# Optimization experiments

Hardware: AMD Instinct MI355X
Metric: run time of the kernel (lower is better)

Reference implementation:

```python
import jax, jax.numpy as jnp
import numpy as np

K = 16          # neighboursnum
NEG_SLOPE = 0.01  # torch LeakyReLU default
EPS = 1e-5      # torch BatchNorm default


def _bn(x, gamma, beta, axes):
    # BatchNorm in training mode: biased batch stats over `axes`, channel dim = 1
    mu = x.mean(axes, keepdims=True)
    var = x.var(axes, keepdims=True)
    shape = [1] * x.ndim
    shape[1] = -1
    return (x - mu) / jnp.sqrt(var + EPS) * gamma.reshape(shape) + beta.reshape(shape)


def _lrelu(x):
    return jnp.where(x >= 0, x, NEG_SLOPE * x)


def setup_inputs() -> dict:
    key = jax.random.key(0)
    ks = jax.random.split(key, 9)
    B, D, N, O = 4, 64, 4096, 128
    s = 0.05
    return {
        "f_in": jax.random.normal(ks[0], (B, D, N), jnp.float32),
        "w_local": jax.random.normal(ks[1], (O, 2 * D + 1), jnp.float32) * s,
        "g_local": jnp.ones((O,), jnp.float32),
        "b_local": jnp.zeros((O,), jnp.float32),
        "w_sem": jax.random.normal(ks[2], (O, D), jnp.float32) * s,
        "g_sem": jnp.ones((O,), jnp.float32),
        "b_sem": jnp.zeros((O,), jnp.float32),
        "w_full": jax.random.normal(ks[3], (O, 2 * O), jnp.float32) * s,
        "g_full": jnp.ones((O,), jnp.float32),
        "b_full": jnp.zeros((O,), jnp.float32),
        "wq": jax.random.normal(ks[4], (D, D), jnp.float32) * s,
        "bq": jax.random.normal(ks[5], (D,), jnp.float32) * s,
        "wk": jax.random.normal(ks[6], (D, D), jnp.float32) * s,
        "bk": jax.random.normal(ks[7], (D,), jnp.float32) * s,
        "wv": jax.random.normal(ks[8], (D, D), jnp.float32) * s,
        "bv": jax.random.normal(jax.random.fold_in(key, 99), (D,), jnp.float32) * s,
    }


def reference(f_in, w_local, g_local, b_local, w_sem, g_sem, b_sem,
              w_full, g_full, b_full, wq, bq, wk, bk, wv, bv):
    B, D, N = f_in.shape
    # --- knn on feature space: pairwise negative squared distance, topk ---
    xx = jnp.sum(f_in * f_in, axis=1)                       # (B,N)
    inner = jnp.einsum('bdm,bdn->bmn', f_in, f_in)          # (B,N,N)
    pd = -xx[:, :, None] + 2.0 * inner - xx[:, None, :]     # -||xi-xj||^2
    idx = jax.lax.top_k(pd, K)[1]                           # (B,N,K) nearest
    # --- gather graph feature ---
    x_t = jnp.swapaxes(f_in, 1, 2)                          # (B,N,D)
    neigh = x_t[jnp.arange(B)[:, None, None], idx]          # (B,N,K,D)
    central = jnp.broadcast_to(x_t[:, :, None, :], neigh.shape)
    dist = jnp.linalg.norm(neigh - central, axis=3, keepdims=True)  # (B,N,K,1)
    feat = jnp.concatenate([central, neigh, dist], axis=3)  # (B,N,K,2D+1)
    feat = jnp.transpose(feat, (0, 3, 1, 2))                # (B,2D+1,N,K)
    # --- localConv (1x1 conv2d, no bias) + BN2d + LeakyReLU, max over K ---
    intra = _lrelu(_bn(jnp.einsum('oc,bcnk->bonk', w_local, feat),
                       g_local, b_local, (0, 2, 3)))
    intra = intra.max(axis=-1)                              # (B,O,N)
    # --- self-attention over points ---
    q = jnp.einsum('od,bdn->bon', wq, f_in) + bq[None, :, None]
    k = jnp.einsum('od,bdn->bon', wk, f_in) + bk[None, :, None]
    v = jnp.einsum('od,bdn->bon', wv, f_in) + bv[None, :, None]
    scores = jax.nn.softmax(
        jnp.einsum('bdm,bdn->bmn', q, k) / jnp.sqrt(jnp.float32(D)), axis=-1)
    fgt = jnp.einsum('bmn,bdn->bdm', scores, v)             # (B,D,N)
    # --- semConv (1x1 conv1d) + BN1d + LeakyReLU ---
    inter = _lrelu(_bn(jnp.einsum('od,bdn->bon', w_sem, fgt),
                       g_sem, b_sem, (0, 2)))               # (B,O,N)
    # --- fullConv on concat ---
    cat = jnp.concatenate([intra, inter], axis=1)           # (B,2O,N)
    out = _lrelu(_bn(jnp.einsum('oc,bcn->bon', w_full, cat),
                     g_full, b_full, (0, 2)))               # (B,O,N)
    return out
```

## Files before the change

kernel.cpp:

```cpp
#include <hip/hip_runtime.h>
#include <math.h>

constexpr int NB = 4;
constexpr int ND = 64;
constexpr int NNN = 4096;
constexpr int NO = 128;
constexpr int NK = 16;
constexpr float NEG = 0.01f;
constexpr float BN_EPS = 1e-5f;

typedef unsigned short u16;
typedef unsigned int u32;
typedef __attribute__((ext_vector_type(8))) short short8;
typedef __attribute__((ext_vector_type(4))) float floatx4;

constexpr int OFF_XX    = 0;
constexpr int OFF_IDX   = 16384;
constexpr int OFF_D2    = 278528;
constexpr int OFF_Q     = 540672;
constexpr int OFF_K     = 1589248;
constexpr int OFF_V     = 2637824;
constexpr int OFF_FGT   = 3686400;
constexpr int OFF_APRE  = 4734976;
constexpr int OFF_BPRE  = 6832128;
constexpr int OFF_IMAX  = 8929280;
constexpr int OFF_IMIN  = 11026432;
constexpr int OFF_ZSEM  = OFF_Q;
constexpr int OFF_ZFULL = OFF_V;
constexpr int OFF_STATS = 13123584;
constexpr int OFF_COEF  = 13124352;
constexpr int OFF_LINV  = 13125120;

__device__ __forceinline__ u16 f2b(float x) {
  u32 u = __builtin_bit_cast(u32, x);
  u += 0x7fffu + ((u >> 16) & 1u);
  return (u16)(u >> 16);
}

template <int CTRL>
__device__ __forceinline__ float fmax_dpp(float v) {
  int b = __builtin_bit_cast(int, v);
  int s = __builtin_amdgcn_update_dpp(b, b, CTRL, 0xF, 0xF, false);
  return fmaxf(v, __builtin_bit_cast(float, s));
}
__device__ __forceinline__ void pairmax(float av, int ai, float bv, int bi, float& rv, int& ri) {
  bool tk = bv > av;
  rv = tk ? bv : av;
  ri = tk ? bi : ai;
}

__global__ void k_xx(const float* __restrict__ f, float* __restrict__ xx) {
  int gid = blockIdx.x * 256 + threadIdx.x;
  int b = gid >> 12, n = gid & 4095;
  const float* fb = f + b * ND * NNN + n;
  float s = 0.f;
#pragma unroll
  for (int d = 0; d < ND; ++d) { float v = fb[d * NNN]; s += v * v; }
  xx[gid] = s;
}

__global__ __launch_bounds__(256) void k_qkv(const float* __restrict__ f,
    const float* __restrict__ wq, const float* __restrict__ bq,
    const float* __restrict__ wk, const float* __restrict__ bk,
    const float* __restrict__ wv, const float* __restrict__ bv,
    u16* __restrict__ qb, u16* __restrict__ kb, u16* __restrict__ vb) {
  int sel = blockIdx.y;
  const float* W    = (sel == 0) ? wq : (sel == 1) ? wk : wv;
  const float* bias = (sel == 0) ? bq : (sel == 1) ? bk : bv;
  int t = threadIdx.x;
  int lane = t & 63;
  int og = __builtin_amdgcn_readfirstlane(t >> 6);
  int gcol = blockIdx.x * 64 + lane;
  int b = gcol >> 12, n = gcol & 4095;
  const float* fb = f + b * ND * NNN + n;
  float cv[64];
#pragma unroll
  for (int d = 0; d < ND; ++d) cv[d] = fb[d * NNN];
  float acc[16];
#pragma unroll 1
  for (int oi = 0; oi < 16; ++oi) {
    int o = og * 16 + oi;
    const float* wr = W + o * ND;
    float a = bias[o];
#pragma unroll
    for (int d = 0; d < ND; ++d) a += wr[d] * cv[d];
    acc[oi] = a;
  }
  if (sel == 2) {
#pragma unroll
    for (int oi = 0; oi < 16; ++oi)
      vb[(size_t)(b * ND + og * 16 + oi) * NNN + n] = f2b(acc[oi]);
  } else {
    short8 p0, p1;
#pragma unroll
    for (int oi = 0; oi < 8; ++oi) { p0[oi] = (short)f2b(acc[oi]); p1[oi] = (short)f2b(acc[8 + oi]); }
    u16* dst = (sel ? kb : qb) + (size_t)(b * NNN + n) * ND + og * 16;
    *(short8*)dst = p0;
    *(short8*)(dst + 8) = p1;
  }
}

__global__ __launch_bounds__(256, 4) void k_knn(const float* __restrict__ f, const float* __restrict__ xx,
                                                int* __restrict__ tidx, float* __restrict__ td2) {
  __shared__ __align__(16) float fm[ND * 8];
  __shared__ __align__(16) float sl[4 * 2048];
  int t = threadIdx.x;
  int lane = t & 63;
  int w = __builtin_amdgcn_readfirstlane(t >> 6);
  int b = blockIdx.x >> 9;
  int m0 = (blockIdx.x & 511) << 3;
  const float* fb = f + b * ND * NNN;
  { int e = t;       int d = e >> 3, r = e & 7; fm[e] = fb[d * NNN + m0 + r]; }
  { int e = t + 256; int d = e >> 3, r = e & 7; fm[e] = fb[d * NNN + m0 + r]; }
  __syncthreads();
  float lv[2][2];
  int   li[2][2];
#pragma unroll
  for (int h = 0; h < 2; ++h) {
    float acc[64];
#pragma unroll
    for (int i = 0; i < 64; ++i) acc[i] = 0.f;
    for (int d = 0; d < ND; ++d) {
      const float* frow = fb + d * NNN + h * 2048 + 4 * t;
      float4 v0 = *(const float4*)(frow);
      float4 v1 = *(const float4*)(frow + 1024);
      float4 r0 = *(const float4*)&fm[d * 8];
      float4 r1 = *(const float4*)&fm[d * 8 + 4];
      float va0[4] = {v0.x, v0.y, v0.z, v0.w};
      float va1[4] = {v1.x, v1.y, v1.z, v1.w};
      float rr[8]  = {r0.x, r0.y, r0.z, r0.w, r1.x, r1.y, r1.z, r1.w};
#pragma unroll
      for (int c2 = 0; c2 < 4; ++c2)
#pragma unroll
        for (int r = 0; r < 8; ++r) {
          acc[c2 * 8 + r]      += va0[c2] * rr[r];
          acc[32 + c2 * 8 + r] += va1[c2] * rr[r];
        }
    }
    {
      const float* xrow = xx + b * NNN + h * 2048 + 4 * t;
      float4 x0 = *(const float4*)(xrow);
      float4 x1 = *(const float4*)(xrow + 1024);
      float xa0[4] = {x0.x, x0.y, x0.z, x0.w};
      float xa1[4] = {x1.x, x1.y, x1.z, x1.w};
#pragma unroll
      for (int c2 = 0; c2 < 4; ++c2)
#pragma unroll
        for (int r = 0; r < 8; ++r) {
          acc[c2 * 8 + r]      = 2.f * acc[c2 * 8 + r]      - xa0[c2];
          acc[32 + c2 * 8 + r] = 2.f * acc[32 + c2 * 8 + r] - xa1[c2];
        }
    }
#pragma unroll
    for (int s = 0; s < 2; ++s) {
      __syncthreads();
#pragma unroll
      for (int r4 = 0; r4 < 4; ++r4) {
        int r = s * 4 + r4;
#pragma unroll
        for (int jj = 0; jj < 2; ++jj) {
          float4 w4;
          w4.x = acc[jj * 32 + 0 * 8 + r];
          w4.y = acc[jj * 32 + 1 * 8 + r];
          w4.z = acc[jj * 32 + 2 * 8 + r];
          w4.w = acc[jj * 32 + 3 * 8 + r];
          *(float4*)&sl[r4 * 2048 + jj * 1024 + 4 * t] = w4;
        }
      }
      __syncthreads();
      float vals[32];
#pragma unroll
      for (int i = 0; i < 32; ++i) vals[i] = sl[w * 2048 + i * 64 + lane];
      float gv[8]; int gi[8];
#pragma unroll
      for (int g = 0; g < 8; ++g) {
        float v0 = vals[g * 4]; int i0 = (g * 4) * 64 + lane;
#pragma unroll
        for (int k2 = 1; k2 < 4; ++k2)
          pairmax(v0, i0, vals[g * 4 + k2], (g * 4 + k2) * 64 + lane, v0, i0);
        gv[g] = v0; gi[g] = i0;
      }
      float t1v[4]; int t1i[4];
      float t2v[2]; int t2i[2];
      float lvv; int lii;
#pragma unroll
      for (int p = 0; p < 4; ++p) pairmax(gv[2 * p], gi[2 * p], gv[2 * p + 1], gi[2 * p + 1], t1v[p], t1i[p]);
#pragma unroll
      for (int q = 0; q < 2; ++q) pairmax(t1v[2 * q], t1i[2 * q], t1v[2 * q + 1], t1i[2 * q + 1], t2v[q], t2i[q]);
      pairmax(t2v[0], t2i[0], t2v[1], t2i[1], lvv, lii);
      float selv = 0.f; int seli = 0;
#pragma unroll 1
      for (int kx = 0; kx < NK; ++kx) {
        float W = lvv;
        W = fmax_dpp<0xB1>(W);
        W = fmax_dpp<0x4E>(W);
        W = fmax_dpp<0x124>(W);
        W = fmax_dpp<0x128>(W);
        W = fmaxf(W, __shfl_xor(W, 16));
        W = fmaxf(W, __shfl_xor(W, 32));
        unsigned long long mk = __ballot(lvv == W);
        int lw = (int)__ffsll(mk) - 1;
        int wcol = __builtin_amdgcn_readlane(lii, lw);
        if (lane == kx) { selv = W; seli = wcol; }
        int jw = wcol >> 6;
#pragma unroll
        for (int g = 0; g < 8; ++g)
          if (g == (jw >> 2)) {
#pragma unroll
            for (int k2 = 0; k2 < 4; ++k2)
              if (k2 == (jw & 3))
                vals[g * 4 + k2] = (lane == lw) ? -3.0e38f : vals[g * 4 + k2];
            float v0 = vals[g * 4]; int i0 = (g * 4) * 64 + lane;
#pragma unroll
            for (int k2 = 1; k2 < 4; ++k2)
              pairmax(v0, i0, vals[g * 4 + k2], (g * 4 + k2) * 64 + lane, v0, i0);
            gv[g] = v0; gi[g] = i0;
            int p = g >> 1;
            pairmax(gv[2 * p], gi[2 * p], gv[2 * p + 1], gi[2 * p + 1], t1v[p], t1i[p]);
            int q = p >> 1;
            pairmax(t1v[2 * q], t1i[2 * q], t1v[2 * q + 1], t1i[2 * q + 1], t2v[q], t2i[q]);
            pairmax(t2v[0], t2i[0], t2v[1], t2i[1], lvv, lii);
          }
      }
      lv[h][s] = selv; li[h][s] = h * 2048 + seli;
    }
  }
#pragma unroll
  for (int s = 0; s < 2; ++s) {
    int m = m0 + s * 4 + w;
    float xm = xx[b * NNN + m];
    float a   = lv[0][s]; int ai  = li[0][s];
    float bb2 = lv[1][s]; int bi2 = li[1][s];
    int cntB = 0, cntA = 0;
#pragma unroll
    for (int j = 0; j < 16; ++j) {
      float bj = __shfl(bb2, j);
      cntB += (bj > a) ? 1 : 0;
      float aj = __shfl(a, j);
      cntA += (aj >= bb2) ? 1 : 0;
    }
    if (lane < 16) {
      int base = (b * NNN + m) * NK;
      int rA = lane + cntB;
      int rB = lane + cntA;
      if (rA < NK) {
        float dd = xm - a;
        tidx[base + rA] = ai;
        td2[base + rA] = dd > 0.f ? dd : 0.f;
      }
      if (rB < NK) {
        float dd = xm - bb2;
        tidx[base + rB] = bi2;
        td2[base + rB] = dd > 0.f ? dd : 0.f;
      }
    }
  }
}

__global__ __launch_bounds__(256) void k_attn(const u16* __restrict__ qb,
                                              const u16* __restrict__ kb,
                                              const u16* __restrict__ vb,
                                              float* __restrict__ fgt,
                                              float* __restrict__ linv) {
  __shared__ __align__(16) u16 P[32 * 520];
  __shared__ float rsum[4][32];
  int t = threadIdx.x;
  int lane = t & 63;
  int w = __builtin_amdgcn_readfirstlane(t >> 6);
  int quad = lane >> 4;
  int l15 = lane & 15;
  int b = blockIdx.x >> 7;
  int m0 = (blockIdx.x & 127) << 5;
  const u16* qra = qb + (size_t)(b * NNN + m0 + l15) * ND + quad * 8;
  const u16* qrb = qb + (size_t)(b * NNN + m0 + 16 + l15) * ND + quad * 8;
  short8 qa0a = *(const short8*)(qra), qa1a = *(const short8*)(qra + 32);
  short8 qa0b = *(const short8*)(qrb), qa1b = *(const short8*)(qrb + 32);
  const u16* kbase = kb + (size_t)b * NNN * ND;
  const u16* vrow  = vb + (size_t)(b * ND + w * 16 + l15) * NNN;
  floatx4 c2a = {0.f, 0.f, 0.f, 0.f};
  floatx4 c2b = {0.f, 0.f, 0.f, 0.f};
  float rsa[4] = {0.f, 0.f, 0.f, 0.f};
  float rsb[4] = {0.f, 0.f, 0.f, 0.f};
#pragma unroll 1
  for (int it = 0; it < 8; ++it) {
    int nchunk = it * 512;
#pragma unroll 1
    for (int ct = 0; ct < 8; ++ct) {
      int cc0 = (w * 8 + ct) * 16;
      const u16* krow = kbase + (size_t)(nchunk + cc0 + l15) * ND + quad * 8;
      short8 kf0 = *(const short8*)(krow);
      short8 kf1 = *(const short8*)(krow + 32);
      floatx4 acca = {0.f, 0.f, 0.f, 0.f};
      acca = __builtin_amdgcn_mfma_f32_16x16x32_bf16(qa0a, kf0, acca, 0, 0, 0);
      acca = __builtin_amdgcn_mfma_f32_16x16x32_bf16(qa1a, kf1, acca, 0, 0, 0);
      floatx4 accb = {0.f, 0.f, 0.f, 0.f};
      accb = __builtin_amdgcn_mfma_f32_16x16x32_bf16(qa0b, kf0, accb, 0, 0, 0);
      accb = __builtin_amdgcn_mfma_f32_16x16x32_bf16(qa1b, kf1, accb, 0, 0, 0);
      int ccol = cc0 + l15;
#pragma unroll
      for (int r = 0; r < 4; ++r) {
        float ea = __expf(acca[r] * 0.125f);
        rsa[r] += ea;
        P[(quad * 4 + r) * 520 + ccol] = f2b(ea);
        float eb = __expf(accb[r] * 0.125f);
        rsb[r] += eb;
        P[(16 + quad * 4 + r) * 520 + ccol] = f2b(eb);
      }
    }
    __syncthreads();
    const u16* vp = vrow + nchunk + quad * 8;
#pragma unroll
    for (int kk = 0; kk < 16; ++kk) {
      short8 b2 = *(const short8*)(vp + kk * 32);
      short8 a2a = *(const short8*)&P[l15 * 520 + kk * 32 + quad * 8];
      short8 a2b = *(const short8*)&P[(16 + l15) * 520 + kk * 32 + quad * 8];
      c2a = __builtin_amdgcn_mfma_f32_16x16x32_bf16(a2a, b2, c2a, 0, 0, 0);
      c2b = __builtin_amdgcn_mfma_f32_16x16x32_bf16(a2b, b2, c2b, 0, 0, 0);
    }
    __syncthreads();
  }
#pragma unroll
  for (int r = 0; r < 4; ++r) {
    float va = rsa[r];
    va += __shfl_xor(va, 1); va += __shfl_xor(va, 2);
    va += __shfl_xor(va, 4); va += __shfl_xor(va, 8);
    rsa[r] = va;
    float vb2 = rsb[r];
    vb2 += __shfl_xor(vb2, 1); vb2 += __shfl_xor(vb2, 2);
    vb2 += __shfl_xor(vb2, 4); vb2 += __shfl_xor(vb2, 8);
    rsb[r] = vb2;
  }
  if (l15 == 0) {
#pragma unroll
    for (int r = 0; r < 4; ++r) {
      rsum[w][quad * 4 + r] = rsa[r];
      rsum[w][16 + quad * 4 + r] = rsb[r];
    }
  }
#pragma unroll
  for (int r = 0; r < 4; ++r) {
    fgt[(size_t)(b * NNN + m0 + quad * 4 + r) * ND + w * 16 + l15] = c2a[r];
    fgt[(size_t)(b * NNN + m0 + 16 + quad * 4 + r) * ND + w * 16 + l15] = c2b[r];
  }
  __syncthreads();
  if (t < 32) {
    float s = rsum[0][t] + rsum[1][t] + rsum[2][t] + rsum[3][t];
    linv[b * NNN + m0 + t] = 1.f / s;
  }
}

__global__ __launch_bounds__(256) void k_ab(const float* __restrict__ f, const float* __restrict__ wl,
                                            float* __restrict__ Apre, float* __restrict__ Bpre) {
  __shared__ float fl[ND * 64];
  int t = threadIdx.x;
  int b = blockIdx.x >> 6;
  int n0 = (blockIdx.x & 63) << 6;
  for (int e = t; e < ND * 64; e += 256) {
    int d = e >> 6, c = e & 63;
    fl[e] = f[b * ND * NNN + d * NNN + n0 + c];
  }
  __syncthreads();
  int lane = t & 63;
  int w = __builtin_amdgcn_readfirstlane(t >> 6);
#pragma unroll 1
  for (int g = 0; g < 8; ++g) {
    float acc[8] = {0, 0, 0, 0, 0, 0, 0, 0};
    int p0 = w * 64 + g * 8;
    for (int d = 0; d < ND; ++d) {
      float fv = fl[d * 64 + lane];
#pragma unroll
      for (int u = 0; u < 8; ++u) {
        int p = p0 + u;
        int o = p & 127, sel = p >> 7;
        acc[u] += wl[o * 129 + sel * 64 + d] * fv;
      }
    }
#pragma unroll
    for (int u = 0; u < 8; ++u) {
      int p = p0 + u;
      int o = p & 127, sel = p >> 7;
      float* outp = sel ? Bpre : Apre;
      outp[(b * NNN + n0 + lane) * NO + o] = acc[u];
    }
  }
}

__global__ __launch_bounds__(128) void k_intra(const float* __restrict__ Apre, const float* __restrict__ Bpre,
                                               const int* __restrict__ tidx, const float* __restrict__ td2,
                                               const float* __restrict__ wl, float* __restrict__ imax,
                                               float* __restrict__ imin, float* __restrict__ stats) {
  __shared__ int sidx[32 * NK];
  __shared__ float sdst[32 * NK];
  int t = threadIdx.x;
  int b = blockIdx.x >> 7;
  int n0 = (blockIdx.x & 127) << 5;
  for (int e = t; e < 32 * NK; e += 128) {
    int base = (b * NNN + n0 + (e >> 4)) * NK + (e & 15);
    sidx[e] = tidx[base];
    sdst[e] = sqrtf(td2[base]);
  }
  __syncthreads();
  int o = t;
  float w128 = wl[o * 129 + 128];
  float ssum = 0.f, ssq = 0.f;
  for (int c = 0; c < 32; ++c) {
    float a = Apre[(b * NNN + n0 + c) * NO + o];
    float mx = -3.4e38f, mn = 3.4e38f;
#pragma unroll
    for (int kx = 0; kx < NK; ++kx) {
      int id = sidx[c * NK + kx];
      float y = a + Bpre[(b * NNN + id) * NO + o] + w128 * sdst[c * NK + kx];
      mx = fmaxf(mx, y); mn = fminf(mn, y);
      ssum += y; ssq += y * y;
    }
    imax[(b * NO + o) * NNN + n0 + c] = mx;
    imin[(b * NO + o) * NNN + n0 + c] = mn;
  }
  atomicAdd(&stats[o], ssum);
  atomicAdd(&stats[NO + o], ssq);
}

__global__ __launch_bounds__(256) void k_sem(const float* __restrict__ fgt, const float* __restrict__ linv,
                                             const float* __restrict__ wsem, float* __restrict__ zsem) {
  __shared__ float fl[64 * 65];
  int t = threadIdx.x;
  int b = blockIdx.x >> 6;
  int n0 = (blockIdx.x & 63) << 6;
  for (int e = t; e < 64 * 64; e += 256) {
    int n = e >> 6, d = e & 63;
    fl[n * 65 + d] = fgt[(size_t)(b * NNN + n0 + n) * ND + d] * linv[b * NNN + n0 + n];
  }
  __syncthreads();
  int lane = t & 63;
  int ob = __builtin_amdgcn_readfirstlane((t >> 6) * 32);
#pragma unroll 1
  for (int g = 0; g < 4; ++g) {
    float acc[8] = {0, 0, 0, 0, 0, 0, 0, 0};
    for (int d = 0; d < ND; ++d) {
      float fv = fl[lane * 65 + d];
#pragma unroll
      for (int u = 0; u < 8; ++u) acc[u] += wsem[(ob + g * 8 + u) * ND + d] * fv;
    }
#pragma unroll
    for (int u = 0; u < 8; ++u)
      zsem[(b * NO + ob + g * 8 + u) * NNN + n0 + lane] = acc[u];
  }
}

__global__ void k_stats(const float* __restrict__ zz, float* __restrict__ sout) {
  int o = blockIdx.x, t = threadIdx.x;
  float s = 0.f, q = 0.f;
  for (int b2 = 0; b2 < NB; ++b2) {
    const float* p = zz + (size_t)(b2 * NO + o) * NNN;
    for (int n = t; n < NNN; n += 256) { float v = p[n]; s += v; q += v * v; }
  }
#pragma unroll
  for (int off = 32; off; off >>= 1) { s += __shfl_down(s, off); q += __shfl_down(q, off); }
  __shared__ float rs[4], rq[4];
  int lane = t & 63, w = t >> 6;
  if (lane == 0) { rs[w] = s; rq[w] = q; }
  __syncthreads();
  if (t == 0) {
    sout[o]      = rs[0] + rs[1] + rs[2] + rs[3];
    sout[NO + o] = rq[0] + rq[1] + rq[2] + rq[3];
  }
}

__global__ void k_fin(const float* __restrict__ stats, const float* __restrict__ g,
                      const float* __restrict__ be, float cnt_inv, float* __restrict__ coef) {
  int o = threadIdx.x;
  float mean = stats[o] * cnt_inv;
  float var = stats[NO + o] * cnt_inv - mean * mean;
  var = var > 0.f ? var : 0.f;
  float a = g[o] * rsqrtf(var + BN_EPS);
  coef[o] = a;
  coef[NO + o] = be[o] - mean * a;
}

__global__ __launch_bounds__(256) void k_full(const float* __restrict__ imax, const float* __restrict__ imin,
                                              const float* __restrict__ zsem, const float* __restrict__ wfull,
                                              const float* __restrict__ coef, float* __restrict__ zfull) {
  __shared__ float fl[2 * NO * 64];
  int t = threadIdx.x;
  int b = blockIdx.x >> 6;
  int n0 = (blockIdx.x & 63) << 6;
  for (int e = t; e < 2 * NO * 64; e += 256) {
    int c = e >> 6, col = e & 63;
    float aa, bb, x;
    if (c < NO) {
      aa = coef[c]; bb = coef[NO + c];
      const float* src = (aa >= 0.f) ? imax : imin;
      x = src[(b * NO + c) * NNN + n0 + col];
    } else {
      int c2 = c - NO;
      aa = coef[2 * NO + c2]; bb = coef[3 * NO + c2];
      x = zsem[(b * NO + c2) * NNN + n0 + col];
    }
    float y = aa * x + bb;
    fl[e] = (y >= 0.f) ? y : NEG * y;
  }
  __syncthreads();
  int lane = t & 63;
  int ob = __builtin_amdgcn_readfirstlane((t >> 6) * 32);
#pragma unroll 1
  for (int g = 0; g < 4; ++g) {
    float acc[8] = {0, 0, 0, 0, 0, 0, 0, 0};
    for (int c = 0; c < 2 * NO; ++c) {
      float fv = fl[c * 64 + lane];
#pragma unroll
      for (int u = 0; u < 8; ++u) acc[u] += wfull[(ob + g * 8 + u) * (2 * NO) + c] * fv;
    }
#pragma unroll
    for (int u = 0; u < 8; ++u)
      zfull[(b * NO + ob + g * 8 + u) * NNN + n0 + lane] = acc[u];
  }
}

__global__ void k_out(const float* __restrict__ zfull, const float* __restrict__ coef,
                      float* __restrict__ out) {
  int gid = blockIdx.x * 256 + threadIdx.x;
  int o = (gid >> 12) & 127;
  float y = coef[o] * zfull[gid] + coef[NO + o];
  out[gid] = (y >= 0.f) ? y : NEG * y;
}

extern "C" void kernel_launch(void* const* d_in, const int* in_sizes, int n_in,
                              void* d_out, int out_size, void* d_ws, size_t ws_size,
                              hipStream_t stream) {
  (void)in_sizes; (void)n_in; (void)out_size; (void)ws_size;
  const float* f       = (const float*)d_in[0];
  const float* w_local = (const float*)d_in[1];
  const float* g_local = (const float*)d_in[2];
  const float* b_local = (const float*)d_in[3];
  const float* w_sem   = (const float*)d_in[4];
  const float* g_sem   = (const float*)d_in[5];
  const float* b_sem   = (const float*)d_in[6];
  const float* w_full  = (const float*)d_in[7];
  const float* g_full  = (const float*)d_in[8];
  const float* b_full  = (const float*)d_in[9];
  const float* wq = (const float*)d_in[10];
  const float* bq = (const float*)d_in[11];
  const float* wk = (const float*)d_in[12];
  const float* bk = (const float*)d_in[13];
  const float* wv = (const float*)d_in[14];
  const float* bv = (const float*)d_in[15];
  float* Wp = (float*)d_ws;
  u16* qb16 = (u16*)(Wp + OFF_Q);
  u16* kb16 = (u16*)(Wp + OFF_K);
  u16* vb16 = (u16*)(Wp + OFF_V);

  hipMemsetAsync(Wp + OFF_STATS, 0, 2 * NO * sizeof(float), stream);
  k_xx  <<<NB * NNN / 256, 256, 0, stream>>>(f, Wp + OFF_XX);
  k_qkv <<<dim3(NB * NNN / 64, 3), 256, 0, stream>>>(f, wq, bq, wk, bk, wv, bv, qb16, kb16, vb16);
  k_knn <<<NB * (NNN / 8), 256, 0, stream>>>(f, Wp + OFF_XX, (int*)(Wp + OFF_IDX), Wp + OFF_D2);
  k_attn<<<NB * (NNN / 32), 256, 0, stream>>>(qb16, kb16, vb16, Wp + OFF_FGT, Wp + OFF_LINV);
  k_ab  <<<NB * (NNN / 64), 256, 0, stream>>>(f, w_local, Wp + OFF_APRE, Wp + OFF_BPRE);
  k_intra<<<NB * (NNN / 32), 128, 0, stream>>>(Wp + OFF_APRE, Wp + OFF_BPRE,
                                               (const int*)(Wp + OFF_IDX), Wp + OFF_D2,
                                               w_local, Wp + OFF_IMAX, Wp + OFF_IMIN, Wp + OFF_STATS);
  k_sem <<<NB * (NNN / 64), 256, 0, stream>>>(Wp + OFF_FGT, Wp + OFF_LINV, w_sem, Wp + OFF_ZSEM);
  k_stats<<<NO, 256, 0, stream>>>(Wp + OFF_ZSEM, Wp + OFF_STATS + 2 * NO);
  k_fin <<<1, NO, 0, stream>>>(Wp + OFF_STATS,          g_local, b_local,
                               1.f / (float)(NB * NNN * NK), Wp + OFF_COEF);
  k_fin <<<1, NO, 0, stream>>>(Wp + OFF_STATS + 2 * NO, g_sem, b_sem,
                               1.f / (float)(NB * NNN), Wp + OFF_COEF + 2 * NO);
  k_full<<<NB * (NNN / 64), 256, 0, stream>>>(Wp + OFF_IMAX, Wp + OFF_IMIN, Wp + OFF_ZSEM,
                                              w_full, Wp + OFF_COEF, Wp + OFF_ZFULL);
  k_stats<<<NO, 256, 0, stream>>>(Wp + OFF_ZFULL, Wp + OFF_STATS + 4 * NO);
  k_fin <<<1, NO, 0, stream>>>(Wp + OFF_STATS + 4 * NO, g_full, b_full,
                               1.f / (float)(NB * NNN), Wp + OFF_COEF + 4 * NO);
  k_out <<<NB * NO * NNN / 256, 256, 0, stream>>>(Wp + OFF_ZFULL, Wp + OFF_COEF + 4 * NO,
                                                  (float*)d_out);
}
```

Before: 650.3 us.

## Fuse BN stats into producer kernels, bf16 A/B precompute, merge QKV and fin launches

Several independent changes. The BN sum and sum-of-squares reductions for the sem and full convolutions move into the producing kernels through wave shuffles and atomics, which removes two k_stats launches and their extra reads of zsem and zfull. The two k_fin launches become a single k_fin2. k_qkv now loops over Q, K and V inside one block so each feature column is loaded once, at the cost of three times fewer blocks. Apre and Bpre are stored as bf16 to halve the gather traffic in k_intra, which adds rounding error to the local-branch activations.

```diff
diff --git a/kernel.cpp b/kernel.cpp
--- a/kernel.cpp
+++ b/kernel.cpp
@@ -36,6 +36,10 @@
   u += 0x7fffu + ((u >> 16) & 1u);
   return (u16)(u >> 16);
 }
+__device__ __forceinline__ float b2f(u16 h) {
+  u32 u = (u32)h << 16;
+  return __builtin_bit_cast(float, u);
+}
 
 template <int CTRL>
 __device__ __forceinline__ float fmax_dpp(float v) {
@@ -64,9 +68,6 @@
     const float* __restrict__ wk, const float* __restrict__ bk,
     const float* __restrict__ wv, const float* __restrict__ bv,
     u16* __restrict__ qb, u16* __restrict__ kb, u16* __restrict__ vb) {
-  int sel = blockIdx.y;
-  const float* W    = (sel == 0) ? wq : (sel == 1) ? wk : wv;
-  const float* bias = (sel == 0) ? bq : (sel == 1) ? bk : bv;
   int t = threadIdx.x;
   int lane = t & 63;
   int og = __builtin_amdgcn_readfirstlane(t >> 6);
@@ -76,27 +77,32 @@
   float cv[64];
 #pragma unroll
   for (int d = 0; d < ND; ++d) cv[d] = fb[d * NNN];
-  float acc[16];
-#pragma unroll 1
-  for (int oi = 0; oi < 16; ++oi) {
-    int o = og * 16 + oi;
-    const float* wr = W + o * ND;
-    float a = bias[o];
-#pragma unroll
-    for (int d = 0; d < ND; ++d) a += wr[d] * cv[d];
-    acc[oi] = a;
-  }
-  if (sel == 2) {
-#pragma unroll
-    for (int oi = 0; oi < 16; ++oi)
-      vb[(size_t)(b * ND + og * 16 + oi) * NNN + n] = f2b(acc[oi]);
-  } else {
-    short8 p0, p1;
-#pragma unroll
-    for (int oi = 0; oi < 8; ++oi) { p0[oi] = (short)f2b(acc[oi]); p1[oi] = (short)f2b(acc[8 + oi]); }
-    u16* dst = (sel ? kb : qb) + (size_t)(b * NNN + n) * ND + og * 16;
-    *(short8*)dst = p0;
-    *(short8*)(dst + 8) = p1;
+#pragma unroll 1
+  for (int sel = 0; sel < 3; ++sel) {
+    const float* W    = (sel == 0) ? wq : (sel == 1) ? wk : wv;
+    const float* bias = (sel == 0) ? bq : (sel == 1) ? bk : bv;
+    float acc[16];
+#pragma unroll 1
+    for (int oi = 0; oi < 16; ++oi) {
+      int o = og * 16 + oi;
+      const float* wr = W + o * ND;
+      float a = bias[o];
+#pragma unroll
+      for (int d = 0; d < ND; ++d) a += wr[d] * cv[d];
+      acc[oi] = a;
+    }
+    if (sel == 2) {
+#pragma unroll
+      for (int oi = 0; oi < 16; ++oi)
+        vb[(size_t)(b * ND + og * 16 + oi) * NNN + n] = f2b(acc[oi]);
+    } else {
+      short8 p0, p1;
+#pragma unroll
+      for (int oi = 0; oi < 8; ++oi) { p0[oi] = (short)f2b(acc[oi]); p1[oi] = (short)f2b(acc[8 + oi]); }
+      u16* dst = (sel ? kb : qb) + (size_t)(b * NNN + n) * ND + og * 16;
+      *(short8*)dst = p0;
+      *(short8*)(dst + 8) = p1;
+    }
   }
 }
 
@@ -350,7 +356,7 @@
 }
 
 __global__ __launch_bounds__(256) void k_ab(const float* __restrict__ f, const float* __restrict__ wl,
-                                            float* __restrict__ Apre, float* __restrict__ Bpre) {
+                                            u16* __restrict__ Apre, u16* __restrict__ Bpre) {
   __shared__ float fl[ND * 64];
   int t = threadIdx.x;
   int b = blockIdx.x >> 6;
@@ -379,13 +385,13 @@
     for (int u = 0; u < 8; ++u) {
       int p = p0 + u;
       int o = p & 127, sel = p >> 7;
-      float* outp = sel ? Bpre : Apre;
-      outp[(b * NNN + n0 + lane) * NO + o] = acc[u];
-    }
-  }
-}
-
-__global__ __launch_bounds__(128) void k_intra(const float* __restrict__ Apre, const float* __restrict__ Bpre,
+      u16* outp = sel ? Bpre : Apre;
+      outp[(size_t)(b * NNN + n0 + lane) * NO + o] = f2b(acc[u]);
+    }
+  }
+}
+
+__global__ __launch_bounds__(128) void k_intra(const u16* __restrict__ Apre, const u16* __restrict__ Bpre,
                                                const int* __restrict__ tidx, const float* __restrict__ td2,
                                                const float* __restrict__ wl, float* __restrict__ imax,
                                                float* __restrict__ imin, float* __restrict__ stats) {
@@ -404,12 +410,12 @@
   float w128 = wl[o * 129 + 128];
   float ssum = 0.f, ssq = 0.f;
   for (int c = 0; c < 32; ++c) {
-    float a = Apre[(b * NNN + n0 + c) * NO + o];
+    float a = b2f(Apre[(size_t)(b * NNN + n0 + c) * NO + o]);
     float mx = -3.4e38f, mn = 3.4e38f;
 #pragma unroll
     for (int kx = 0; kx < NK; ++kx) {
       int id = sidx[c * NK + kx];
-      float y = a + Bpre[(b * NNN + id) * NO + o] + w128 * sdst[c * NK + kx];
+      float y = a + b2f(Bpre[(size_t)(b * NNN + id) * NO + o]) + w128 * sdst[c * NK + kx];
       mx = fmaxf(mx, y); mn = fminf(mn, y);
       ssum += y; ssq += y * y;
     }
@@ -421,7 +427,8 @@
 }
 
 __global__ __launch_bounds__(256) void k_sem(const float* __restrict__ fgt, const float* __restrict__ linv,
-                                             const float* __restrict__ wsem, float* __restrict__ zsem) {
+                                             const float* __restrict__ wsem, float* __restrict__ zsem,
+                                             float* __restrict__ sout) {
   __shared__ float fl[64 * 65];
   int t = threadIdx.x;
   int b = blockIdx.x >> 6;
@@ -442,28 +449,34 @@
       for (int u = 0; u < 8; ++u) acc[u] += wsem[(ob + g * 8 + u) * ND + d] * fv;
     }
 #pragma unroll
-    for (int u = 0; u < 8; ++u)
-      zsem[(b * NO + ob + g * 8 + u) * NNN + n0 + lane] = acc[u];
-  }
-}
-
-__global__ void k_stats(const float* __restrict__ zz, float* __restrict__ sout) {
-  int o = blockIdx.x, t = threadIdx.x;
-  float s = 0.f, q = 0.f;
-  for (int b2 = 0; b2 < NB; ++b2) {
-    const float* p = zz + (size_t)(b2 * NO + o) * NNN;
-    for (int n = t; n < NNN; n += 256) { float v = p[n]; s += v; q += v * v; }
-  }
-#pragma unroll
-  for (int off = 32; off; off >>= 1) { s += __shfl_down(s, off); q += __shfl_down(q, off); }
-  __shared__ float rs[4], rq[4];
-  int lane = t & 63, w = t >> 6;
-  if (lane == 0) { rs[w] = s; rq[w] = q; }
-  __syncthreads();
-  if (t == 0) {
-    sout[o]      = rs[0] + rs[1] + rs[2] + rs[3];
-    sout[NO + o] = rq[0] + rq[1] + rq[2] + rq[3];
-  }
+    for (int u = 0; u < 8; ++u) {
+      int o = ob + g * 8 + u;
+      zsem[(b * NO + o) * NNN + n0 + lane] = acc[u];
+      float s = acc[u], q = acc[u] * acc[u];
+#pragma unroll
+      for (int off = 1; off < 64; off <<= 1) { s += __shfl_xor(s, off); q += __shfl_xor(q, off); }
+      if (lane == 0) { atomicAdd(&sout[o], s); atomicAdd(&sout[NO + o], q); }
+    }
+  }
+}
+
+__global__ void k_fin2(const float* __restrict__ stats,
+                       const float* __restrict__ g1, const float* __restrict__ be1, float ci1,
+                       const float* __restrict__ g2, const float* __restrict__ be2, float ci2,
+                       float* __restrict__ coef) {
+  int t = threadIdx.x;
+  int o = t & 127;
+  int which = t >> 7;
+  const float* st = stats + which * 2 * NO;
+  const float* g  = which ? g2 : g1;
+  const float* be = which ? be2 : be1;
+  float ci = which ? ci2 : ci1;
+  float mean = st[o] * ci;
+  float var = st[NO + o] * ci - mean * mean;
+  var = var > 0.f ? var : 0.f;
+  float a = g[o] * rsqrtf(var + BN_EPS);
+  coef[which * 2 * NO + o] = a;
+  coef[which * 2 * NO + NO + o] = be[o] - mean * a;
 }
 
 __global__ void k_fin(const float* __restrict__ stats, const float* __restrict__ g,
@@ -479,7 +492,8 @@
 
 __global__ __launch_bounds__(256) void k_full(const float* __restrict__ imax, const float* __restrict__ imin,
                                               const float* __restrict__ zsem, const float* __restrict__ wfull,
-                                              const float* __restrict__ coef, float* __restrict__ zfull) {
+                                              const float* __restrict__ coef, float* __restrict__ zfull,
+                                              float* __restrict__ sout) {
   __shared__ float fl[2 * NO * 64];
   int t = threadIdx.x;
   int b = blockIdx.x >> 6;
@@ -511,8 +525,14 @@
       for (int u = 0; u < 8; ++u) acc[u] += wfull[(ob + g * 8 + u) * (2 * NO) + c] * fv;
     }
 #pragma unroll
-    for (int u = 0; u < 8; ++u)
-      zfull[(b * NO + ob + g * 8 + u) * NNN + n0 + lane] = acc[u];
+    for (int u = 0; u < 8; ++u) {
+      int o = ob + g * 8 + u;
+      zfull[(b * NO + o) * NNN + n0 + lane] = acc[u];
+      float s = acc[u], q = acc[u] * acc[u];
+#pragma unroll
+      for (int off = 1; off < 64; off <<= 1) { s += __shfl_xor(s, off); q += __shfl_xor(q, off); }
+      if (lane == 0) { atomicAdd(&sout[o], s); atomicAdd(&sout[NO + o], q); }
+    }
   }
 }
 
@@ -548,25 +568,27 @@
   u16* qb16 = (u16*)(Wp + OFF_Q);
   u16* kb16 = (u16*)(Wp + OFF_K);
   u16* vb16 = (u16*)(Wp + OFF_V);
-
-  hipMemsetAsync(Wp + OFF_STATS, 0, 2 * NO * sizeof(float), stream);
+  u16* ap16 = (u16*)(Wp + OFF_APRE);
+  u16* bp16 = (u16*)(Wp + OFF_BPRE);
+
+  hipMemsetAsync(Wp + OFF_STATS, 0, 6 * NO * sizeof(float), stream);
   k_xx  <<<NB * NNN / 256, 256, 0, stream>>>(f, Wp + OFF_XX);
-  k_qkv <<<dim3(NB * NNN / 64, 3), 256, 0, stream>>>(f, wq, bq, wk, bk, wv, bv, qb16, kb16, vb16);
+  k_qkv <<<NB * NNN / 64, 256, 0, stream>>>(f, wq, bq, wk, bk, wv, bv, qb16, kb16, vb16);
   k_knn <<<NB * (NNN / 8), 256, 0, stream>>>(f, Wp + OFF_XX, (int*)(Wp + OFF_IDX), Wp + OFF_D2);
   k_attn<<<NB * (NNN / 32), 256, 0, stream>>>(qb16, kb16, vb16, Wp + OFF_FGT, Wp + OFF_LINV);
-  k_ab  <<<NB * (NNN / 64), 256, 0, stream>>>(f, w_local, Wp + OFF_APRE, Wp + OFF_BPRE);
-  k_intra<<<NB * (NNN / 32), 128, 0, stream>>>(Wp + OFF_APRE, Wp + OFF_BPRE,
+  k_ab  <<<NB * (NNN / 64), 256, 0, stream>>>(f, w_local, ap16, bp16);
+  k_intra<<<NB * (NNN / 32), 128, 0, stream>>>(ap16, bp16,
                                                (const int*)(Wp + OFF_IDX), Wp + OFF_D2,
                                                w_local, Wp + OFF_IMAX, Wp + OFF_IMIN, Wp + OFF_STATS);
-  k_sem <<<NB * (NNN / 64), 256, 0, stream>>>(Wp + OFF_FGT, Wp + OFF_LINV, w_sem, Wp + OFF_ZSEM);
-  k_stats<<<NO, 256, 0, stream>>>(Wp + OFF_ZSEM, Wp + OFF_STATS + 2 * NO);
-  k_fin <<<1, NO, 0, stream>>>(Wp + OFF_STATS,          g_local, b_local,
-                               1.f / (float)(NB * NNN * NK), Wp + OFF_COEF);
-  k_fin <<<1, NO, 0, stream>>>(Wp + OFF_STATS + 2 * NO, g_sem, b_sem,
-                               1.f / (float)(NB * NNN), Wp + OFF_COEF + 2 * NO);
+  k_sem <<<NB * (NNN / 64), 256, 0, stream>>>(Wp + OFF_FGT, Wp + OFF_LINV, w_sem, Wp + OFF_ZSEM,
+                                              Wp + OFF_STATS + 2 * NO);
+  k_fin2<<<1, 2 * NO, 0, stream>>>(Wp + OFF_STATS,
+                                   g_local, b_local, 1.f / (float)(NB * NNN * NK),
+                                   g_sem, b_sem, 1.f / (float)(NB * NNN),
+                                   Wp + OFF_COEF);
   k_full<<<NB * (NNN / 64), 256, 0, stream>>>(Wp + OFF_IMAX, Wp + OFF_IMIN, Wp + OFF_ZSEM,
-                                              w_full, Wp + OFF_COEF, Wp + OFF_ZFULL);
-  k_stats<<<NO, 256, 0, stream>>>(Wp + OFF_ZFULL, Wp + OFF_STATS + 4 * NO);
+                                              w_full, Wp + OFF_COEF, Wp + OFF_ZFULL,
+                                              Wp + OFF_STATS + 4 * NO);
   k_fin <<<1, NO, 0, stream>>>(Wp + OFF_STATS + 4 * NO, g_full, b_full,
                                1.f / (float)(NB * NNN), Wp + OFF_COEF + 4 * NO);
   k_out <<<NB * NO * NNN / 256, 256, 0, stream>>>(Wp + OFF_ZFULL, Wp + OFF_COEF + 4 * NO,
```

New measurement: 773.6 us. 1.19x slower.
